# Kernel tuning notes

Hardware: AMD Instinct MI355X
Metric: run time of the kernel (lower is better)

Reference implementation:

```python
import jax, jax.numpy as jnp
import numpy as np

N_NODES = 100000
N_EDGES = 3200000
D_FEAT = 256
K_MAX = 5
NEG_SLOPE = 0.2


def _segment_softmax(e, seg, n):
    m = jax.ops.segment_max(e, seg, num_segments=n)
    ex = jnp.exp(e - m[seg])
    s = jax.ops.segment_sum(ex, seg, num_segments=n)
    return ex / (s[seg] + 1e-16)


def setup_inputs() -> dict:
    key = jax.random.key(0)
    ks = jax.random.split(key, 8)
    x = jax.random.normal(ks[0], (N_NODES, D_FEAT), dtype=jnp.float32)
    pos = jax.random.normal(ks[1], (N_NODES, 3), dtype=jnp.float32)
    w_l = jax.random.normal(ks[2], (D_FEAT, 1), dtype=jnp.float32) / np.sqrt(D_FEAT)
    w_r = jax.random.normal(ks[3], (D_FEAT, 1), dtype=jnp.float32) / np.sqrt(D_FEAT)
    w_e = jax.random.normal(ks[4], (3, 1), dtype=jnp.float32)
    att = jax.random.normal(ks[5], (1,), dtype=jnp.float32)
    bias = jnp.zeros((1,), dtype=jnp.float32)
    edge_index = jax.random.randint(ks[6], (2, N_EDGES), 0, N_NODES, dtype=jnp.int64)
    return {"x": x, "pos": pos, "w_l": w_l, "w_r": w_r, "w_e": w_e,
            "att": att, "bias": bias, "edge_index": edge_index}


def reference(x, pos, w_l, w_r, w_e, att, bias, edge_index):
    src, dst = edge_index[0], edge_index[1]
    n = x.shape[0]
    # GATv2Conv (heads=1, out_channels=1) scoring
    xl = x @ w_l                                  # [N,1] source transform
    xr = x @ w_r                                  # [N,1] target transform
    ea = (pos[dst] - pos[src]) @ w_e              # [E,1] edge-attr transform
    msg = xl[src] + xr[dst] + ea                  # [E,1]
    e = (jax.nn.leaky_relu(msg, NEG_SLOPE) * att).sum(-1)  # [E]
    alpha = _segment_softmax(e, dst, n)           # attention over incoming edges
    out = jax.ops.segment_sum(alpha[:, None] * xl[src], dst, num_segments=n) + bias
    logits = out[:, 0]                            # [N]
    score = jax.nn.softmax(logits)                # global node score

    # select highest-score node, grow k-hop neighborhood (<= k_max hops)
    node_id = jnp.argmax(jax.lax.stop_gradient(score))
    reach = jnp.zeros((n,), dtype=bool).at[node_id].set(True)
    for _ in range(K_MAX):
        frontier = jax.ops.segment_max(reach[src].astype(jnp.int32), dst,
                                       num_segments=n) > 0
        reach = reach | frontier
    reach = jax.lax.stop_gradient(reach)

    # pool_val = max over neighborhood features (Neighborhood.pool_val)
    pooled = jnp.max(jnp.where(reach[:, None], x, -jnp.inf), axis=0)  # [D]
    return jnp.concatenate([score, pooled])
```

## Files before the change

### kernel.cpp

```cpp
#include <hip/hip_runtime.h>

#define D_FEAT 256
#define NEG_SLOPE 0.2f
#define MAXBINS 512
#define SENT 0xFFFFFFFFu

__device__ __forceinline__ unsigned fmap(float f) {
    unsigned u = __float_as_uint(f);
    return (u & 0x80000000u) ? ~u : (u | 0x80000000u);
}
__device__ __forceinline__ float funmap(unsigned u) {
    return __uint_as_float((u & 0x80000000u) ? (u ^ 0x80000000u) : ~u);
}
__device__ __forceinline__ float dot4(float4 v, float4 w) {
    return v.x * w.x + v.y * w.y + v.z * w.z + v.w * w.w;
}


__global__ void k_pre(const float* __restrict__ x, const float* __restrict__ w_l,
                      const float* __restrict__ w_r, const float* __restrict__ pos,
                      const float* __restrict__ w_e,
                      float2* __restrict__ sA, float* __restrict__ Bv,
                      float4* __restrict__ gABpart, unsigned* __restrict__ stampW,
                      unsigned* __restrict__ gHist, unsigned* __restrict__ sc,
                      int n, int nW) {
    int blk = blockIdx.x, tid = threadIdx.x;
    int gid = blk * 256 + tid;
    if (gid < nW) stampW[gid] = 0xFFFFFFFFu;
    if (blk == 0) {
        if (tid < MAXBINS) gHist[tid] = 0u;
        if (tid + 256 < MAXBINS) gHist[tid + 256] = 0u;
        if (tid == 0) sc[8] = 0u;
    }
    int w = tid >> 6, lane = tid & 63;
    int node0 = blk * 16 + w * 4;
    float4 al = ((const float4*)w_l)[lane];
    float4 bl = ((const float4*)w_r)[lane];
    float sl0 = 0.f, sl1 = 0.f, sl2 = 0.f, sl3 = 0.f;
    float sr0 = 0.f, sr1 = 0.f, sr2 = 0.f, sr3 = 0.f;
    if (node0 + 3 < n) {
        float4 v0 = ((const float4*)(x + (size_t)node0 * D_FEAT))[lane];
        float4 v1 = ((const float4*)(x + (size_t)(node0 + 1) * D_FEAT))[lane];
        float4 v2 = ((const float4*)(x + (size_t)(node0 + 2) * D_FEAT))[lane];
        float4 v3 = ((const float4*)(x + (size_t)(node0 + 3) * D_FEAT))[lane];
        sl0 = dot4(v0, al); sr0 = dot4(v0, bl);
        sl1 = dot4(v1, al); sr1 = dot4(v1, bl);
        sl2 = dot4(v2, al); sr2 = dot4(v2, bl);
        sl3 = dot4(v3, al); sr3 = dot4(v3, bl);
    } else if (node0 < n) {
        {
            float4 v = ((const float4*)(x + (size_t)node0 * D_FEAT))[lane];
            sl0 = dot4(v, al); sr0 = dot4(v, bl);
        }
        if (node0 + 1 < n) {
            float4 v = ((const float4*)(x + (size_t)(node0 + 1) * D_FEAT))[lane];
            sl1 = dot4(v, al); sr1 = dot4(v, bl);
        }
        if (node0 + 2 < n) {
            float4 v = ((const float4*)(x + (size_t)(node0 + 2) * D_FEAT))[lane];
            sl2 = dot4(v, al); sr2 = dot4(v, bl);
        }
    }
    #pragma unroll
    for (int o = 32; o; o >>= 1) {
        sl0 += __shfl_xor(sl0, o); sr0 += __shfl_xor(sr0, o);
        sl1 += __shfl_xor(sl1, o); sr1 += __shfl_xor(sr1, o);
        sl2 += __shfl_xor(sl2, o); sr2 += __shfl_xor(sr2, o);
        sl3 += __shfl_xor(sl3, o); sr3 += __shfl_xor(sr3, o);
    }
    float amax = -INFINITY, bmaxv = -INFINITY, amin = INFINITY, bminv = INFINITY;
    int node = node0 + lane;
    if (lane < 4 && node < n) {
        float slv = (lane == 0) ? sl0 : (lane == 1) ? sl1 : (lane == 2) ? sl2 : sl3;
        float srv = (lane == 0) ? sr0 : (lane == 1) ? sr1 : (lane == 2) ? sr2 : sr3;
        float p = pos[3 * node] * w_e[0] + pos[3 * node + 1] * w_e[1]
                + pos[3 * node + 2] * w_e[2];
        float a = slv - p, b = srv + p;
        sA[node] = make_float2(a, slv);
        Bv[node] = b;
        amax = a; amin = a; bmaxv = b; bminv = b;
    }
    #pragma unroll
    for (int o = 1; o < 4; o <<= 1) {
        amax = fmaxf(amax, __shfl_xor(amax, o));
        bmaxv = fmaxf(bmaxv, __shfl_xor(bmaxv, o));
        amin = fminf(amin, __shfl_xor(amin, o));
        bminv = fminf(bminv, __shfl_xor(bminv, o));
    }
    __shared__ float s4[4][4];
    if (lane == 0) { s4[w][0] = amax; s4[w][1] = bmaxv; s4[w][2] = amin; s4[w][3] = bminv; }
    __syncthreads();
    if (tid == 0) {
        float AM = s4[0][0], BM = s4[0][1], Am = s4[0][2], Bm = s4[0][3];
        #pragma unroll
        for (int k = 1; k < 4; ++k) {
            AM = fmaxf(AM, s4[k][0]); BM = fmaxf(BM, s4[k][1]);
            Am = fminf(Am, s4[k][2]); Bm = fminf(Bm, s4[k][3]);
        }
        gABpart[blk] = make_float4(AM, BM, Am, Bm);
    }
}

__global__ void k_hist(const int4* __restrict__ dst4, int E4, int nbins,
                       unsigned* __restrict__ gHist) {
    __shared__ unsigned h[MAXBINS];
    for (int b = threadIdx.x; b < nbins; b += blockDim.x) h[b] = 0u;
    __syncthreads();
    int stride = gridDim.x * blockDim.x;
    for (int i = blockIdx.x * blockDim.x + threadIdx.x; i < E4; i += stride) {
        int4 d = dst4[i];
        atomicAdd(&h[d.x >> 8], 1u);
        atomicAdd(&h[d.y >> 8], 1u);
        atomicAdd(&h[d.z >> 8], 1u);
        atomicAdd(&h[d.w >> 8], 1u);
    }
    __syncthreads();
    for (int b = threadIdx.x; b < nbins; b += blockDim.x)
        if (h[b]) atomicAdd(&gHist[b], h[b]);
}

__global__ void k_scan2(const float4* __restrict__ gABpart, int nAB,
                        const unsigned* __restrict__ gHist,
                        unsigned* __restrict__ gBase, unsigned* __restrict__ gCursor,
                        int nbins, int nBlk, unsigned* sc, const float* __restrict__ att) {
    int tid = threadIdx.x;
    float AM = -INFINITY, BM = -INFINITY, Am = INFINITY, Bm = INFINITY;
    for (int i = tid; i < nAB; i += 256) {
        float4 v = gABpart[i];
        AM = fmaxf(AM, v.x); BM = fmaxf(BM, v.y);
        Am = fminf(Am, v.z); Bm = fminf(Bm, v.w);
    }
    #pragma unroll
    for (int o = 32; o; o >>= 1) {
        AM = fmaxf(AM, __shfl_xor(AM, o)); BM = fmaxf(BM, __shfl_xor(BM, o));
        Am = fminf(Am, __shfl_xor(Am, o)); Bm = fminf(Bm, __shfl_xor(Bm, o));
    }
    __shared__ float s4[4][4];
    int w = tid >> 6, lane = tid & 63;
    if (lane == 0) { s4[w][0] = AM; s4[w][1] = BM; s4[w][2] = Am; s4[w][3] = Bm; }
    __syncthreads();
    if (tid == 0) {
        float am = s4[0][0], bm = s4[0][1], an = s4[0][2], bn = s4[0][3];
        #pragma unroll
        for (int k = 1; k < 4; ++k) {
            am = fmaxf(am, s4[k][0]); bm = fmaxf(bm, s4[k][1]);
            an = fminf(an, s4[k][2]); bn = fminf(bn, s4[k][3]);
        }
        float at = att[0];
        float z = (at >= 0.f) ? (am + bm) : (an + bn);
        float lz = (z >= 0.f) ? z : NEG_SLOPE * z;
        ((float*)sc)[3] = lz * at;
        sc[0] = 0u; ((float*)sc)[1] = 0.f; sc[2] = 0xFFFFFFFFu;
    }
    __syncthreads();
    if (tid < 64) {
        unsigned padw = 15u * (unsigned)nBlk;
        unsigned carry = 0;
        for (int b0 = 0; b0 < nbins; b0 += 64) {
            int b = b0 + tid;
            unsigned v = (b < nbins) ? ((gHist[b] + padw + 15u) & ~15u) : 0u;
            unsigned inc = v;
            #pragma unroll
            for (int o = 1; o < 64; o <<= 1) {
                unsigned t = __shfl_up(inc, o);
                if (tid >= o) inc += t;
            }
            unsigned excl = inc - v + carry;
            if (b < nbins) { gBase[b] = excl; gCursor[b] = excl; }
            carry += __shfl(inc, 63);
        }
    }
}

__global__ void k_scatter(const int4* __restrict__ src4, const int4* __restrict__ dst4,
                          unsigned* __restrict__ gCursor, unsigned* __restrict__ recs,
                          int E4, int nbins) {
    __shared__ unsigned h[MAXBINS];
    __shared__ unsigned base[MAXBINS];
    for (int b = threadIdx.x; b < nbins; b += 512) h[b] = 0u;
    __syncthreads();
    int b4 = blockIdx.x * 2048;
    #pragma unroll
    for (int g = 0; g < 4; ++g) {
        int idx = b4 + g * 512 + threadIdx.x;
        if (idx < E4) {
            int4 d = dst4[idx];
            atomicAdd(&h[d.x >> 8], 1u);
            atomicAdd(&h[d.y >> 8], 1u);
            atomicAdd(&h[d.z >> 8], 1u);
            atomicAdd(&h[d.w >> 8], 1u);
        }
    }
    __syncthreads();
    for (int b = threadIdx.x; b < nbins; b += 512) {
        unsigned c = h[b];
        h[b] = 0u;
        base[b] = c ? atomicAdd(&gCursor[b], (c + 15u) & ~15u) : 0u;
    }
    __syncthreads();
    #pragma unroll
    for (int g = 0; g < 4; ++g) {
        int idx = b4 + g * 512 + threadIdx.x;
        if (idx < E4) {
            int4 sv = src4[idx];
            int4 dv = dst4[idx];
            int ss[4] = { sv.x, sv.y, sv.z, sv.w };
            int dd[4] = { dv.x, dv.y, dv.z, dv.w };
            #pragma unroll
            for (int j = 0; j < 4; ++j) {
                int d_ = dd[j];
                int bin = d_ >> 8;
                unsigned off = atomicAdd(&h[bin], 1u);
                recs[base[bin] + off] = (unsigned)ss[j] | ((unsigned)(d_ & 255) << 17);
            }
        }
    }
    __syncthreads();
    for (int b = threadIdx.x; b < nbins; b += 512) {
        unsigned c = h[b];
        unsigned pc = (c + 15u) & ~15u;
        for (unsigned k = c; k < pc; ++k) recs[base[b] + k] = SENT;
    }
}

__global__ void k_binsum(const uint4* __restrict__ recs4, const unsigned* __restrict__ gBase,
                         const unsigned* __restrict__ gCursor,
                         const float2* __restrict__ sA, const float* __restrict__ Bv,
                         const float* __restrict__ att, const float* __restrict__ bias,
                         float* __restrict__ logits, unsigned* sc, int n) {
    __shared__ float accx[256];
    __shared__ float accy[256];
    __shared__ float Bb[256];
    int b = blockIdx.x;
    int tid = threadIdx.x;
    int node0 = b << 8;
    accx[tid] = 0.f; accy[tid] = 0.f;
    Bb[tid] = (node0 + tid < n) ? Bv[node0 + tid] : 0.f;
    __syncthreads();
    const float at = att[0];
    const float M = ((const float*)sc)[3];
    unsigned q0 = gBase[b] >> 2, q1 = gCursor[b] >> 2;
    for (unsigned i = q0 + tid; i < q1; i += 256u) {
        uint4 r4 = recs4[i];
        unsigned ws[4] = { r4.x, r4.y, r4.z, r4.w };
        #pragma unroll
        for (int j = 0; j < 4; ++j) {
            unsigned wv = ws[j];
            if (wv == SENT) continue;
            int sidx = (int)(wv & 0x1FFFFu);
            int loc  = (int)(wv >> 17);
            float2 sa = sA[sidx];
            float msg = sa.x + Bb[loc];
            float lr = (msg >= 0.f) ? msg : NEG_SLOPE * msg;
            float e = expf(lr * at - M);
            atomicAdd(&accx[loc], e);
            atomicAdd(&accy[loc], e * sa.y);
        }
    }
    __syncthreads();
    int node = node0 + tid;
    float lg = -INFINITY;
    if (node < n) {
        lg = accy[tid] / (accx[tid] + 1e-38f) + bias[0];
        logits[node] = lg;
    }
    unsigned mu = fmap(lg);
    #pragma unroll
    for (int o = 32; o; o >>= 1) { unsigned t = __shfl_xor(mu, o); mu = (t > mu) ? t : mu; }
    __shared__ unsigned wm[4];
    int w_ = tid >> 6, l = tid & 63;
    if (l == 0) wm[w_] = mu;
    __syncthreads();
    if (tid == 0) {
        unsigned m = wm[0];
        #pragma unroll
        for (int k = 1; k < 4; ++k) m = (wm[k] > m) ? wm[k] : m;
        atomicMax(&sc[0], m);
    }
}


__global__ void k_sumarg(float* __restrict__ logits, unsigned* sc, int n) {
    int i = blockIdx.x * blockDim.x + threadIdx.x;
    unsigned gmax_u = sc[0];
    float gmax = funmap(gmax_u);
    float ex = 0.f;
    if (i < n) {
        float lg = logits[i];
        ex = expf(lg - gmax);
        if (fmap(lg) == gmax_u) atomicMin(&sc[2], (unsigned)i);
        logits[i] = ex;
    }
    #pragma unroll
    for (int o = 32; o; o >>= 1) ex += __shfl_xor(ex, o);
    if ((threadIdx.x & 63) == 0) atomicAdd((float*)&sc[1], ex);
}

__global__ void k_score(const float* __restrict__ logits, const unsigned* __restrict__ sc,
                        float* __restrict__ out, unsigned char* stamp, int n) {
    int i = blockIdx.x * blockDim.x + threadIdx.x;
    if (i >= n) return;
    float gsum = ((const float*)sc)[1];
    out[i] = logits[i] / gsum;
    if (i == (int)sc[2]) stamp[i] = 0;
}

__global__ void k_bfs_stamp(const int4* __restrict__ src4, const int4* __restrict__ dst4,
                            unsigned char* __restrict__ stamp, int E4, int t) {
    int i = blockIdx.x * blockDim.x + threadIdx.x;
    if (i >= E4) return;
    int4 s = src4[i];
    unsigned char th = (unsigned char)t;
    bool h0 = stamp[s.x] < th;
    bool h1 = stamp[s.y] < th;
    bool h2 = stamp[s.z] < th;
    bool h3 = stamp[s.w] < th;
    if (!(h0 | h1 | h2 | h3)) return;
    int4 d = dst4[i];
    if (h0 && stamp[d.x] > th) stamp[d.x] = th;
    if (h1 && stamp[d.y] > th) stamp[d.y] = th;
    if (h2 && stamp[d.z] > th) stamp[d.z] = th;
    if (h3 && stamp[d.w] > th) stamp[d.w] = th;
}

__global__ void k_pool1(const float* __restrict__ x, const unsigned char* __restrict__ stamp,
                        float4* __restrict__ partial, int n) {
    int sub = threadIdx.x >> 6;
    int lane = threadIdx.x & 63;
    float4 m = make_float4(-INFINITY, -INFINITY, -INFINITY, -INFINITY);
    int stride = gridDim.x * 4;
    for (int node = blockIdx.x * 4 + sub; node < n; node += stride) {
        if (stamp[node] != 0xFF) {
            float4 v = ((const float4*)(x + (size_t)node * D_FEAT))[lane];
            m.x = fmaxf(m.x, v.x); m.y = fmaxf(m.y, v.y);
            m.z = fmaxf(m.z, v.z); m.w = fmaxf(m.w, v.w);
        }
    }
    __shared__ float4 red[256];
    red[threadIdx.x] = m;
    __syncthreads();
    if (sub == 0) {
        float4 a = red[lane], b = red[64 + lane], c = red[128 + lane], d = red[192 + lane];
        a.x = fmaxf(fmaxf(a.x, b.x), fmaxf(c.x, d.x));
        a.y = fmaxf(fmaxf(a.y, b.y), fmaxf(c.y, d.y));
        a.z = fmaxf(fmaxf(a.z, b.z), fmaxf(c.z, d.z));
        a.w = fmaxf(fmaxf(a.w, b.w), fmaxf(c.w, d.w));
        partial[(size_t)blockIdx.x * 64 + lane] = a;
    }
}

__global__ void k_pool2g(const float4* __restrict__ partial, int nblk1,
                         float4* __restrict__ partial2, unsigned* sc,
                         float* __restrict__ out, int n) {
    int sub = threadIdx.x >> 6;
    int lane = threadIdx.x & 63;
    int chunk = (nblk1 + gridDim.x - 1) / gridDim.x;
    int b0 = blockIdx.x * chunk;
    int b1 = min(b0 + chunk, nblk1);
    float4 m = make_float4(-INFINITY, -INFINITY, -INFINITY, -INFINITY);
    for (int b = b0 + sub; b < b1; b += 4) {
        float4 v = partial[(size_t)b * 64 + lane];
        m.x = fmaxf(m.x, v.x); m.y = fmaxf(m.y, v.y);
        m.z = fmaxf(m.z, v.z); m.w = fmaxf(m.w, v.w);
    }
    __shared__ float4 red[256];
    red[threadIdx.x] = m;
    __syncthreads();
    if (sub == 0) {
        float4 a = red[lane], b = red[64 + lane], c = red[128 + lane], d = red[192 + lane];
        a.x = fmaxf(fmaxf(a.x, b.x), fmaxf(c.x, d.x));
        a.y = fmaxf(fmaxf(a.y, b.y), fmaxf(c.y, d.y));
        a.z = fmaxf(fmaxf(a.z, b.z), fmaxf(c.z, d.z));
        a.w = fmaxf(fmaxf(a.w, b.w), fmaxf(c.w, d.w));
        partial2[(size_t)blockIdx.x * 64 + lane] = a;
    }
    __threadfence();
    __shared__ unsigned done;
    if (threadIdx.x == 0) done = atomicAdd(&sc[8], 1u);
    __syncthreads();
    if (done != (unsigned)(gridDim.x - 1)) return;
    __threadfence();
    float4 m2 = make_float4(-INFINITY, -INFINITY, -INFINITY, -INFINITY);
    for (int r = sub; r < (int)gridDim.x; r += 4) {
        float4 v = partial2[(size_t)r * 64 + lane];
        m2.x = fmaxf(m2.x, v.x); m2.y = fmaxf(m2.y, v.y);
        m2.z = fmaxf(m2.z, v.z); m2.w = fmaxf(m2.w, v.w);
    }
    __syncthreads();
    red[threadIdx.x] = m2;
    __syncthreads();
    if (sub == 0) {
        float4 a = red[lane], b = red[64 + lane], c = red[128 + lane], d = red[192 + lane];
        a.x = fmaxf(fmaxf(a.x, b.x), fmaxf(c.x, d.x));
        a.y = fmaxf(fmaxf(a.y, b.y), fmaxf(c.y, d.y));
        a.z = fmaxf(fmaxf(a.z, b.z), fmaxf(c.z, d.z));
        a.w = fmaxf(fmaxf(a.w, b.w), fmaxf(c.w, d.w));
        out[n + 4 * lane + 0] = a.x;
        out[n + 4 * lane + 1] = a.y;
        out[n + 4 * lane + 2] = a.z;
        out[n + 4 * lane + 3] = a.w;
    }
}


__global__ void k_init(float2* NS, unsigned* stampW, int nW, unsigned* pooled_u,
                       unsigned* sc, int n) {
    int i = blockIdx.x * blockDim.x + threadIdx.x;
    if (i < n) NS[i] = make_float2(0.f, 0.f);
    if (i < nW) stampW[i] = 0xFFFFFFFFu;
    if (i < D_FEAT) pooled_u[i] = 0u;
    if (i == 0) {
        sc[0] = 0u; ((float*)sc)[1] = 0.f; sc[2] = 0xFFFFFFFFu;
        sc[4] = 0u; sc[5] = 0u; sc[6] = 0xFFFFFFFFu; sc[7] = 0xFFFFFFFFu;
    }
}

__global__ void k_dots(const float* __restrict__ x, const float* __restrict__ w_l,
                       const float* __restrict__ w_r, float* __restrict__ xl,
                       float* __restrict__ xr, int n) {
    int wave = (int)((blockIdx.x * blockDim.x + threadIdx.x) >> 6);
    int lane = threadIdx.x & 63;
    if (wave >= n) return;
    const float4* xv = (const float4*)(x + (size_t)wave * D_FEAT);
    float4 v = xv[lane];
    float4 a = ((const float4*)w_l)[lane];
    float4 b = ((const float4*)w_r)[lane];
    float sl = dot4(v, a);
    float sr = dot4(v, b);
    #pragma unroll
    for (int o = 32; o; o >>= 1) { sl += __shfl_xor(sl, o); sr += __shfl_xor(sr, o); }
    if (lane == 0) { xl[wave] = sl; xr[wave] = sr; }
}

__global__ void k_ab(const float* __restrict__ xl, const float* __restrict__ xr,
                     const float* __restrict__ pos, const float* __restrict__ w_e,
                     float2* __restrict__ sA, float* __restrict__ B,
                     unsigned* sc, int n) {
    int i = blockIdx.x * blockDim.x + threadIdx.x;
    float amax, amin, bmax, bmin;
    if (i < n) {
        float p = pos[3 * i] * w_e[0] + pos[3 * i + 1] * w_e[1] + pos[3 * i + 2] * w_e[2];
        float xli = xl[i];
        float a = xli - p;
        float b = xr[i] + p;
        sA[i] = make_float2(a, xli);
        B[i] = b;
        amax = amin = a; bmax = bmin = b;
    } else {
        amax = bmax = -INFINITY; amin = bmin = INFINITY;
    }
    #pragma unroll
    for (int o = 32; o; o >>= 1) {
        amax = fmaxf(amax, __shfl_xor(amax, o));
        bmax = fmaxf(bmax, __shfl_xor(bmax, o));
        amin = fminf(amin, __shfl_xor(amin, o));
        bmin = fminf(bmin, __shfl_xor(bmin, o));
    }
    __shared__ float s4[4][4];
    int w = threadIdx.x >> 6, l = threadIdx.x & 63;
    if (l == 0) { s4[w][0] = amax; s4[w][1] = bmax; s4[w][2] = amin; s4[w][3] = bmin; }
    __syncthreads();
    if (threadIdx.x == 0) {
        float AM = s4[0][0], BM = s4[0][1], Am = s4[0][2], Bm = s4[0][3];
        #pragma unroll
        for (int k = 1; k < 4; ++k) {
            AM = fmaxf(AM, s4[k][0]); BM = fmaxf(BM, s4[k][1]);
            Am = fminf(Am, s4[k][2]); Bm = fminf(Bm, s4[k][3]);
        }
        atomicMax(&sc[4], fmap(AM)); atomicMax(&sc[5], fmap(BM));
        atomicMin(&sc[6], fmap(Am)); atomicMin(&sc[7], fmap(Bm));
    }
}

__global__ void k_scanM(unsigned* sc, const float* __restrict__ att) {
    if (threadIdx.x == 0) {
        float at = att[0];
        float z = (at >= 0.f) ? (funmap(sc[4]) + funmap(sc[5]))
                              : (funmap(sc[6]) + funmap(sc[7]));
        float lz = (z >= 0.f) ? z : NEG_SLOPE * z;
        ((float*)sc)[3] = lz * at;
        sc[0] = 0u; ((float*)sc)[1] = 0.f; sc[2] = 0xFFFFFFFFu;
    }
}

__global__ void k_edge_sum(const int* __restrict__ src, const int* __restrict__ dst,
                           const float2* __restrict__ sA, const float* __restrict__ B,
                           const float* __restrict__ att, const unsigned* __restrict__ sc,
                           float2* NS, int E) {
    int i = blockIdx.x * blockDim.x + threadIdx.x;
    if (i >= E) return;
    int s = src[i], d = dst[i];
    float2 sa = sA[s];
    float msg = sa.x + B[d];
    float lr = (msg >= 0.f) ? msg : NEG_SLOPE * msg;
    float ex = expf(lr * att[0] - ((const float*)sc)[3]);
    atomicAdd(&NS[d].x, ex);
    atomicAdd(&NS[d].y, ex * sa.y);
}

__global__ void k_logits(const float2* __restrict__ NS, const float* __restrict__ bias,
                         float* __restrict__ logits, unsigned* sc, int n) {
    int i = blockIdx.x * blockDim.x + threadIdx.x;
    unsigned mu = 0u;
    if (i < n) {
        float2 ns = NS[i];
        float lg = ns.y / (ns.x + 1e-38f) + bias[0];
        logits[i] = lg;
        mu = fmap(lg);
    }
    #pragma unroll
    for (int o = 32; o; o >>= 1) { unsigned t = __shfl_xor(mu, o); mu = (t > mu) ? t : mu; }
    if ((threadIdx.x & 63) == 0) atomicMax(&sc[0], mu);
}

__global__ void k_pool2(const float4* __restrict__ partial, int nblk1, unsigned* pooled_u) {
    int sub = threadIdx.x >> 6;
    int lane = threadIdx.x & 63;
    int chunk = (nblk1 + gridDim.x - 1) / gridDim.x;
    int b0 = blockIdx.x * chunk;
    int b1 = min(b0 + chunk, nblk1);
    float4 m = make_float4(-INFINITY, -INFINITY, -INFINITY, -INFINITY);
    for (int b = b0 + sub; b < b1; b += 4) {
        float4 v = partial[(size_t)b * 64 + lane];
        m.x = fmaxf(m.x, v.x); m.y = fmaxf(m.y, v.y);
        m.z = fmaxf(m.z, v.z); m.w = fmaxf(m.w, v.w);
    }
    __shared__ float4 red[256];
    red[threadIdx.x] = m;
    __syncthreads();
    if (sub == 0) {
        float4 a = red[lane], b = red[64 + lane], c = red[128 + lane], d = red[192 + lane];
        a.x = fmaxf(fmaxf(a.x, b.x), fmaxf(c.x, d.x));
        a.y = fmaxf(fmaxf(a.y, b.y), fmaxf(c.y, d.y));
        a.z = fmaxf(fmaxf(a.z, b.z), fmaxf(c.z, d.z));
        a.w = fmaxf(fmaxf(a.w, b.w), fmaxf(c.w, d.w));
        atomicMax(&pooled_u[lane * 4 + 0], fmap(a.x));
        atomicMax(&pooled_u[lane * 4 + 1], fmap(a.y));
        atomicMax(&pooled_u[lane * 4 + 2], fmap(a.z));
        atomicMax(&pooled_u[lane * 4 + 3], fmap(a.w));
    }
}

__global__ void k_poolwrite(const unsigned* __restrict__ pooled_u, float* __restrict__ out, int n) {
    int t = threadIdx.x;
    out[n + t] = funmap(pooled_u[t]);
}

extern "C" void kernel_launch(void* const* d_in, const int* in_sizes, int n_in,
                              void* d_out, int out_size, void* d_ws, size_t ws_size,
                              hipStream_t stream) {
    const float* x    = (const float*)d_in[0];
    const float* pos  = (const float*)d_in[1];
    const float* w_l  = (const float*)d_in[2];
    const float* w_r  = (const float*)d_in[3];
    const float* w_e  = (const float*)d_in[4];
    const float* att  = (const float*)d_in[5];
    const float* bias = (const float*)d_in[6];
    const int*   ei   = (const int*)d_in[7];

    const int n = in_sizes[0] / D_FEAT;
    const int E = in_sizes[7] / 2;
    const int* src = ei;
    const int* dst = ei + E;
    const int nbins = (n + 255) >> 8;
    const int nW = (n + 3) / 4;
    const int nBlkScat = (E + 8191) / 8192;
    const int Bk = 256;
    const int gN  = (n + Bk - 1) / Bk;
    const int gE  = (E + Bk - 1) / Bk;
    const int gD  = (n + 3) / 4;
    const int gP  = (n + 15) / 16;
    const int E4  = E / 4;
    const int gE4 = (E4 + Bk - 1) / Bk;
    const int POOLB = 2048;
    const int POOL2B = 16;

    float* f0 = (float*)d_ws;
    size_t o = 0;
    float*    xl       = f0 + o; o += (size_t)n;
    float*    xr       = f0 + o; o += (size_t)n;
    float2*   sA       = (float2*)(f0 + o); o += 2 * (size_t)n;
    float*    B        = f0 + o; o += (size_t)n;
    float*    logits   = f0 + o; o += (size_t)n;
    o = (o + 3) & ~(size_t)3;
    float2*   NS       = (float2*)(f0 + o); o += 2 * (size_t)n;
    float4*   partialF = (float4*)NS;
    unsigned* stampW   = (unsigned*)(f0 + o); o += (size_t)nW;
    unsigned char* stamp = (unsigned char*)stampW;
    unsigned* pooled_u = (unsigned*)(f0 + o); o += 256;
    unsigned* sc       = (unsigned*)(f0 + o); o += 64;
    unsigned* gBase    = (unsigned*)(f0 + o); o += MAXBINS;
    unsigned* gCursor  = (unsigned*)(f0 + o); o += MAXBINS;
    unsigned* gHist    = (unsigned*)(f0 + o); o += MAXBINS;
    o = (o + 3) & ~(size_t)3;
    float4*   gABpart  = (float4*)(f0 + o); o += 4 * (size_t)gP;
    o = (o + 15) & ~(size_t)15;
    unsigned* recs     = (unsigned*)(f0 + o);
    float4*   partialT = (float4*)recs;
    float4*   partial2 = (float4*)(recs + (size_t)POOLB * 256);

    size_t capWords = (size_t)E + (size_t)nbins * (15u * (size_t)nBlkScat + 16u);
    size_t poolWords = (size_t)POOLB * 256 + (size_t)POOL2B * 256;
    if (poolWords > capWords) capWords = poolWords;
    size_t need_bytes = (o + capWords) * sizeof(float);
    const bool sorted_ok = (ws_size >= need_bytes) && (nbins <= MAXBINS) &&
                           (E % 4 == 0) && (n <= (1 << 17));

    float* out = (float*)d_out;

    if (sorted_ok) {
        k_pre<<<gP, Bk, 0, stream>>>(x, w_l, w_r, pos, w_e, sA, B, gABpart,
                                     stampW, gHist, sc, n, nW);
        k_hist<<<512, Bk, 0, stream>>>((const int4*)dst, E4, nbins, gHist);
        k_scan2<<<1, Bk, 0, stream>>>(gABpart, gP, gHist, gBase, gCursor,
                                      nbins, nBlkScat, sc, att);
        k_scatter<<<nBlkScat, 512, 0, stream>>>((const int4*)src, (const int4*)dst,
                                                gCursor, recs, E4, nbins);
        k_binsum<<<nbins, Bk, 0, stream>>>((const uint4*)recs, gBase, gCursor, sA, B,
                                           att, bias, logits, sc, n);
        k_sumarg<<<gN, Bk, 0, stream>>>(logits, sc, n);
        k_score<<<gN, Bk, 0, stream>>>(logits, sc, out, stamp, n);
        for (int t = 1; t <= 5; ++t) {
            k_bfs_stamp<<<gE4, Bk, 0, stream>>>((const int4*)src, (const int4*)dst,
                                                stamp, E4, t);
        }
        k_pool1<<<POOLB, Bk, 0, stream>>>(x, stamp, partialT, n);
        k_pool2g<<<POOL2B, Bk, 0, stream>>>(partialT, POOLB, partial2, sc, out, n);
    } else {
        k_init<<<gN, Bk, 0, stream>>>(NS, stampW, nW, pooled_u, sc, n);
        k_dots<<<gD, Bk, 0, stream>>>(x, w_l, w_r, xl, xr, n);
        k_ab<<<gN, Bk, 0, stream>>>(xl, xr, pos, w_e, sA, B, sc, n);
        k_scanM<<<1, 64, 0, stream>>>(sc, att);
        k_edge_sum<<<gE, Bk, 0, stream>>>(src, dst, sA, B, att, sc, NS, E);
        k_logits<<<gN, Bk, 0, stream>>>(NS, bias, logits, sc, n);
        k_sumarg<<<gN, Bk, 0, stream>>>(logits, sc, n);
        k_score<<<gN, Bk, 0, stream>>>(logits, sc, out, stamp, n);
        for (int t = 1; t <= 5; ++t) {
            k_bfs_stamp<<<gE4, Bk, 0, stream>>>((const int4*)src, (const int4*)dst,
                                                stamp, E4, t);
        }
        int nblk1 = (int)((2 * (size_t)n) / 256);
        if (nblk1 > 768) nblk1 = 768;
        if (nblk1 < 1) nblk1 = 1;
        k_pool1<<<nblk1, Bk, 0, stream>>>(x, stamp, partialF, n);
        k_pool2<<<16, Bk, 0, stream>>>(partialF, nblk1, pooled_u);
        k_poolwrite<<<1, Bk, 0, stream>>>(pooled_u, out, n);
    }
}
```

Baseline: 264.5 us.

## Fuse scan into histogram via last-block, use dst-sorted records for final BFS hop

The single-block scan kernel is merged into the histogram kernel: the last block to finish, found with an atomic counter, performs the min/max reduction and the scan, which removes one launch. The fifth BFS hop replaces the edge-wise stamp pass with a pull-style kernel over the dst-bucketed records. That kernel skips whole 256-node bins that have no unreached node and otherwise reads only records for its own bin. A quick skip of all-sentinel uint4 records is also added in binsum. The cost is extra synchronisation complexity, and the last-block scan runs serially after the histogram's global atomics.

```diff
diff --git a/kernel.cpp b/kernel.cpp
--- a/kernel.cpp
+++ b/kernel.cpp
@@ -30,7 +30,7 @@
     if (blk == 0) {
         if (tid < MAXBINS) gHist[tid] = 0u;
         if (tid + 256 < MAXBINS) gHist[tid + 256] = 0u;
-        if (tid == 0) sc[8] = 0u;
+        if (tid == 0) { sc[8] = 0u; sc[9] = 0u; }
     }
     int w = tid >> 6, lane = tid & 63;
     int node0 = blk * 16 + w * 4;
@@ -102,12 +102,16 @@
 }
 
 __global__ void k_hist(const int4* __restrict__ dst4, int E4, int nbins,
-                       unsigned* __restrict__ gHist) {
+                       unsigned* __restrict__ gHist,
+                       const float4* __restrict__ gABpart, int nAB,
+                       unsigned* __restrict__ gBase, unsigned* __restrict__ gCursor,
+                       int nBlk, unsigned* sc, const float* __restrict__ att) {
     __shared__ unsigned h[MAXBINS];
-    for (int b = threadIdx.x; b < nbins; b += blockDim.x) h[b] = 0u;
+    int tid = threadIdx.x;
+    for (int b = tid; b < nbins; b += blockDim.x) h[b] = 0u;
     __syncthreads();
     int stride = gridDim.x * blockDim.x;
-    for (int i = blockIdx.x * blockDim.x + threadIdx.x; i < E4; i += stride) {
+    for (int i = blockIdx.x * blockDim.x + tid; i < E4; i += stride) {
         int4 d = dst4[i];
         atomicAdd(&h[d.x >> 8], 1u);
         atomicAdd(&h[d.y >> 8], 1u);
@@ -115,15 +119,14 @@
         atomicAdd(&h[d.w >> 8], 1u);
     }
     __syncthreads();
-    for (int b = threadIdx.x; b < nbins; b += blockDim.x)
+    for (int b = tid; b < nbins; b += blockDim.x)
         if (h[b]) atomicAdd(&gHist[b], h[b]);
-}
-
-__global__ void k_scan2(const float4* __restrict__ gABpart, int nAB,
-                        const unsigned* __restrict__ gHist,
-                        unsigned* __restrict__ gBase, unsigned* __restrict__ gCursor,
-                        int nbins, int nBlk, unsigned* sc, const float* __restrict__ att) {
-    int tid = threadIdx.x;
+    __threadfence();
+    __shared__ unsigned done;
+    if (tid == 0) done = atomicAdd(&sc[9], 1u);
+    __syncthreads();
+    if (done != (unsigned)(gridDim.x - 1)) return;
+    __threadfence();
     float AM = -INFINITY, BM = -INFINITY, Am = INFINITY, Bm = INFINITY;
     for (int i = tid; i < nAB; i += 256) {
         float4 v = gABpart[i];
@@ -242,6 +245,7 @@
     unsigned q0 = gBase[b] >> 2, q1 = gCursor[b] >> 2;
     for (unsigned i = q0 + tid; i < q1; i += 256u) {
         uint4 r4 = recs4[i];
+        if (r4.x == SENT) continue;
         unsigned ws[4] = { r4.x, r4.y, r4.z, r4.w };
         #pragma unroll
         for (int j = 0; j < 4; ++j) {
@@ -321,6 +325,41 @@
     if (h1 && stamp[d.y] > th) stamp[d.y] = th;
     if (h2 && stamp[d.z] > th) stamp[d.z] = th;
     if (h3 && stamp[d.w] > th) stamp[d.w] = th;
+}
+
+__global__ void k_bfs_rec(const uint4* __restrict__ recs4, const unsigned* __restrict__ gBase,
+                          const unsigned* __restrict__ gCursor,
+                          unsigned char* __restrict__ stamp, int n, int t) {
+    __shared__ unsigned char st[256];
+    __shared__ unsigned char mark[256];
+    __shared__ unsigned char wn[4];
+    int b = blockIdx.x;
+    int tid = threadIdx.x;
+    int node = (b << 8) + tid;
+    unsigned char th = (unsigned char)t;
+    unsigned char s = (node < n) ? stamp[node] : (unsigned char)0;
+    st[tid] = s; mark[tid] = 0;
+    unsigned long long ball = __ballot(s > th);
+    if ((tid & 63) == 0) wn[tid >> 6] = (ball != 0ull) ? 1 : 0;
+    __syncthreads();
+    if (!(wn[0] | wn[1] | wn[2] | wn[3])) return;
+    unsigned q0 = gBase[b] >> 2, q1 = gCursor[b] >> 2;
+    for (unsigned i = q0 + tid; i < q1; i += 256u) {
+        uint4 r4 = recs4[i];
+        if (r4.x == SENT) continue;
+        unsigned ws[4] = { r4.x, r4.y, r4.z, r4.w };
+        #pragma unroll
+        for (int j = 0; j < 4; ++j) {
+            unsigned wv = ws[j];
+            if (wv == SENT) continue;
+            int loc = (int)(wv >> 17);
+            if (st[loc] > th) {
+                if (stamp[wv & 0x1FFFFu] < th) mark[loc] = 1;
+            }
+        }
+    }
+    __syncthreads();
+    if (mark[tid] && node < n && st[tid] > th) stamp[node] = th;
 }
 
 __global__ void k_pool1(const float* __restrict__ x, const unsigned char* __restrict__ stamp,
@@ -611,19 +650,21 @@
     if (sorted_ok) {
         k_pre<<<gP, Bk, 0, stream>>>(x, w_l, w_r, pos, w_e, sA, B, gABpart,
                                      stampW, gHist, sc, n, nW);
-        k_hist<<<512, Bk, 0, stream>>>((const int4*)dst, E4, nbins, gHist);
-        k_scan2<<<1, Bk, 0, stream>>>(gABpart, gP, gHist, gBase, gCursor,
-                                      nbins, nBlkScat, sc, att);
+        k_hist<<<512, Bk, 0, stream>>>((const int4*)dst, E4, nbins, gHist,
+                                       gABpart, gP, gBase, gCursor,
+                                       nBlkScat, sc, att);
         k_scatter<<<nBlkScat, 512, 0, stream>>>((const int4*)src, (const int4*)dst,
                                                 gCursor, recs, E4, nbins);
         k_binsum<<<nbins, Bk, 0, stream>>>((const uint4*)recs, gBase, gCursor, sA, B,
                                            att, bias, logits, sc, n);
         k_sumarg<<<gN, Bk, 0, stream>>>(logits, sc, n);
         k_score<<<gN, Bk, 0, stream>>>(logits, sc, out, stamp, n);
-        for (int t = 1; t <= 5; ++t) {
+        for (int t = 1; t <= 4; ++t) {
             k_bfs_stamp<<<gE4, Bk, 0, stream>>>((const int4*)src, (const int4*)dst,
                                                 stamp, E4, t);
         }
+        k_bfs_rec<<<nbins, Bk, 0, stream>>>((const uint4*)recs, gBase, gCursor,
+                                            stamp, n, 5);
         k_pool1<<<POOLB, Bk, 0, stream>>>(x, stamp, partialT, n);
         k_pool2g<<<POOL2B, Bk, 0, stream>>>(partialT, POOLB, partial2, sc, out, n);
     } else {
```

After: 278.0 us. 1.05x slower.
